# Performance work log

Hardware: AMD Instinct MI355X
Metric: run time of the kernel (lower is better)

The kernel has to match this reference:

```python
import jax, jax.numpy as jnp
import numpy as np
import math

BLOCK_SIZE = 64
GATE_HIDDEN = 128


def _rmsnorm(x, w, eps=1e-6):
    v = jnp.mean(jnp.square(x), axis=-1, keepdims=True)
    return x * jax.lax.rsqrt(v + eps) * w


def _rotate_half(x):
    x1, x2 = jnp.split(x, 2, axis=-1)
    return jnp.concatenate([-x2, x1], axis=-1)


def _rope(x, cos, sin):
    # x: [B, S, H, D]; cos/sin: [B, S, D] -> unsqueeze head dim (unsqueeze_dim=2)
    c = cos[:, :, None, :]
    s = sin[:, :, None, :]
    return x * c + _rotate_half(x) * s


def setup_inputs() -> dict:
    key = jax.random.key(0)
    ks = jax.random.split(key, 10)
    B, S, Hk, D = 4, 65536, 8, 128
    Hq, g, Dg = 32, 4, GATE_HIDDEN
    nb = S // BLOCK_SIZE
    xav_q = math.sqrt(6.0 / (D + Dg))
    xav_k = math.sqrt(6.0 / (2 * D + Dg))
    return {
        "k": jax.random.normal(ks[0], (B, S, Hk, D), jnp.float32),
        "q": jax.random.normal(ks[1], (B, 1, Hq, D), jnp.float32),
        "Wq": jax.random.uniform(ks[2], (Hk, g, D, Dg), jnp.float32, -xav_q, xav_q),
        "Wk": jax.random.uniform(ks[3], (Hk, 2 * D, Dg), jnp.float32, -xav_k, xav_k),
        "qnorm_w": jnp.ones((Dg,), jnp.float32),
        "knorm_w": jnp.ones((Dg,), jnp.float32),
        "cos_q": jax.random.uniform(ks[4], (B, 1, Dg), jnp.float32, -1.0, 1.0),
        "sin_q": jax.random.uniform(ks[5], (B, 1, Dg), jnp.float32, -1.0, 1.0),
        "cos_k": jax.random.uniform(ks[6], (B, nb, Dg), jnp.float32, -1.0, 1.0),
        "sin_k": jax.random.uniform(ks[7], (B, nb, Dg), jnp.float32, -1.0, 1.0),
        "attention_mask": jnp.ones((B, Hk, nb), jnp.bool_),
        "block_budget": 128,
    }


def reference(k, q, Wq, Wk, qnorm_w, knorm_w, cos_q, sin_q, cos_k, sin_k,
              attention_mask, block_budget):
    B, S, Hk, D = k.shape
    nb = S // BLOCK_SIZE
    g = q.shape[2] // Hk
    Dg = Wk.shape[-1]
    scale = 1.0 / math.sqrt(Dg)

    # --- K path: block pooling (avg + max) -> per-head linear -> RMSNorm -> RoPE
    kb = k.reshape(B, nb, BLOCK_SIZE, Hk, D)
    k_pooled = jnp.concatenate([kb.mean(axis=2), kb.max(axis=2)], axis=-1)  # [B,nb,Hk,2D]
    k_c = jnp.einsum('bshi,hio->bsho', k_pooled, Wk)                         # [B,nb,Hk,Dg]
    k_c = _rmsnorm(k_c, knorm_w)
    k_c = _rope(k_c, cos_k, sin_k)

    # --- Q path (Qproj): grouped per-k-head projection -> RMSNorm -> RoPE
    qg = q.reshape(B, 1, Hk, g, D)
    qp = jnp.einsum('bskgi,kgio->bsko', qg, Wq)                              # [B,1,Hk,Dg]
    qp = _rmsnorm(qp, qnorm_w)
    qp = _rope(qp, cos_q, sin_q)
    qv = qp[:, 0]                                                            # [B,Hk,Dg]

    # --- gate scores + softmax
    attn = jnp.einsum('bhd,bshd->bhs', qv, k_c) * scale                      # [B,Hk,nb]
    attn = jnp.where(attention_mask, attn, jnp.float32(-1e20))
    attn = jax.nn.softmax(attn, axis=-1)

    # --- token_budget sparse block mask: topk + scatter
    _, topk_idx = jax.lax.top_k(attn, block_budget)                          # [B,Hk,k]
    blk = jnp.arange(nb)
    mask = jnp.any(topk_idx[..., :, None] == blk[None, None, None, :], axis=-2)
    mask = mask & attention_mask
    mask = mask.at[:, :, -1].set(True)
    return mask
```

## Files before the change

### kernel.cpp

```cpp
#include <hip/hip_runtime.h>
#include <hip/hip_bf16.h>
#include <math.h>

#define NB   1024
#define HKH  8
#define NPROD 512

typedef float f4 __attribute__((ext_vector_type(4)));

__global__ __launch_bounds__(512) void qproj_kernel(const float* __restrict__ q,
                                                    const float* __restrict__ Wq,
                                                    const float* __restrict__ qnw,
                                                    const float* __restrict__ cq,
                                                    const float* __restrict__ sq,
                                                    float* __restrict__ qv) {
    int b = blockIdx.x >> 3, h = blockIdx.x & 7;
    int t = threadIdx.x;
    int o = t & 127, seg = t >> 7;
    __shared__ float qs[512];
    __shared__ float part[4][128];
    __shared__ float red[2];
    __shared__ float ybuf[128];
    qs[t] = q[(size_t)b * 4096 + (size_t)h * 512 + t];
    __syncthreads();
    const float* wqp = Wq + (size_t)h * 512 * 128 + o;
    float acc = 0.0f;
    int g0 = seg * 128;
#pragma unroll 4
    for (int gi = g0; gi < g0 + 128; ++gi)
        acc = fmaf(qs[gi], wqp[(size_t)gi * 128], acc);
    part[seg][o] = acc;
    __syncthreads();
    if (t < 128) {
        float a = part[0][o] + part[1][o] + part[2][o] + part[3][o];
        ybuf[o] = a;
        float ss = a * a;
        for (int off = 32; off > 0; off >>= 1) ss += __shfl_xor(ss, off);
        if ((o & 63) == 0) red[o >> 6] = ss;
    }
    __syncthreads();
    if (t < 128) {
        float scale = rsqrtf((red[0] + red[1]) * (1.0f / 128.0f) + 1e-6f);
        float y  = ybuf[o] * scale * qnw[o];
        int op   = (o < 64) ? o + 64 : o - 64;
        float yp = ybuf[op] * scale * qnw[op];
        float rot = (o < 64) ? -yp : yp;
        qv[((size_t)b * HKH + h) * 128 + o] =
            fmaf(y, cq[b * 128 + o], rot * sq[b * 128 + o]);
    }
}

__global__ __launch_bounds__(768) void fused_kernel(const float* __restrict__ kin,
                                                    const float* __restrict__ Wk,
                                                    const float* __restrict__ knw,
                                                    const float* __restrict__ cosk,
                                                    const float* __restrict__ sink,
                                                    const float* __restrict__ qv,
                                                    float* __restrict__ scores) {
    __shared__ float At[4][256][32];
    __shared__ int produced[4];
    int wg  = blockIdx.x;
    int b   = wg >> 6;
    int grp = wg & 63;
    int t   = threadIdx.x;

    if (t < 4) produced[t] = 0;
    __syncthreads();

    if (t < NPROD) {
        int col = t & 255;
        int h   = col >> 5;
        int c   = col & 31;
        int bihalf = t >> 8;
        const float inv = 1.0f / 64.0f;
        for (int it = 0; it < 4; ++it) {
#pragma unroll
            for (int bb2 = 0; bb2 < 2; ++bb2) {
                int bi = bihalf + bb2 * 2;
                size_t row0 = (size_t)b * 65536 +
                              ((size_t)grp * 16 + it * 4 + bi) * 64;
                const f4* src = (const f4*)kin + row0 * 256 + col;
                f4 s = {0.f, 0.f, 0.f, 0.f};
                f4 m = {-3.4e38f, -3.4e38f, -3.4e38f, -3.4e38f};
#pragma unroll 8
                for (int r = 0; r < 64; ++r) {
                    f4 u = __builtin_nontemporal_load(src + (size_t)r * 256);
                    s += u;
                    m.x = fmaxf(m.x, u.x); m.y = fmaxf(m.y, u.y);
                    m.z = fmaxf(m.z, u.z); m.w = fmaxf(m.w, u.w);
                }
#pragma unroll
                for (int j = 0; j < 4; ++j) {
                    int k0 = c * 4 + j;
                    int g  = (k0 >> 3) & 7;
                    At[it][k0      ][((h ^ g) << 2) | bi] = s[j] * inv;
                    At[it][k0 + 128][((h ^ g) << 2) | bi] = m[j];
                }
            }
            __threadfence_block();
            atomicAdd(&produced[it], 1);
        }
    } else {
        int tc = t - NPROD;
        int h  = tc >> 5;
        int c  = tc & 31;
        const float* wp = Wk + (size_t)h * 32768 + c * 4;
        f4 kn  = *(const f4*)(knw + c * 4);
        f4 qvr = *(const f4*)(qv + ((size_t)b * HKH + h) * 128 + c * 4);
        volatile int* vfl = (volatile int*)produced;

#pragma unroll
        for (int pass = 0; pass < 2; ++pass) {
            int sA = pass * 2, sB = sA + 1;
            while (vfl[sB] < NPROD) __builtin_amdgcn_s_sleep(2);
            __threadfence_block();

            float acc0[4][4], acc1[4][4];
#pragma unroll
            for (int i = 0; i < 4; ++i)
#pragma unroll
                for (int j = 0; j < 4; ++j) { acc0[i][j] = 0.0f; acc1[i][j] = 0.0f; }

#pragma unroll 4
            for (int k = 0; k < 256; ++k) {
                int g = (k >> 3) & 7;
                f4 w  = *(const f4*)(wp + (size_t)k * 128);
                f4 a0 = *(const f4*)&At[sA][k][(h ^ g) << 2];
                f4 a1 = *(const f4*)&At[sB][k][(h ^ g) << 2];
#pragma unroll
                for (int i = 0; i < 4; ++i) {
                    acc0[i][0] = fmaf(a0[i], w.x, acc0[i][0]);
                    acc0[i][1] = fmaf(a0[i], w.y, acc0[i][1]);
                    acc0[i][2] = fmaf(a0[i], w.z, acc0[i][2]);
                    acc0[i][3] = fmaf(a0[i], w.w, acc0[i][3]);
                    acc1[i][0] = fmaf(a1[i], w.x, acc1[i][0]);
                    acc1[i][1] = fmaf(a1[i], w.y, acc1[i][1]);
                    acc1[i][2] = fmaf(a1[i], w.z, acc1[i][2]);
                    acc1[i][3] = fmaf(a1[i], w.w, acc1[i][3]);
                }
            }

#pragma unroll
            for (int half = 0; half < 2; ++half) {
                float (*acc)[4] = half ? acc1 : acc0;
#pragma unroll
                for (int i = 0; i < 4; ++i) {
                    int blkg = grp * 16 + (sA + half) * 4 + i;
                    float ss = 0.0f;
#pragma unroll
                    for (int j = 0; j < 4; ++j) ss = fmaf(acc[i][j], acc[i][j], ss);
#pragma unroll
                    for (int off = 1; off < 32; off <<= 1) ss += __shfl_xor(ss, off);
                    float scale = rsqrtf(ss * (1.0f / 128.0f) + 1e-6f);
                    f4 cb = *(const f4*)(cosk + ((size_t)b * NB + blkg) * 128 + c * 4);
                    f4 sb = *(const f4*)(sink + ((size_t)b * NB + blkg) * 128 + c * 4);
                    float part = 0.0f;
#pragma unroll
                    for (int j = 0; j < 4; ++j) {
                        float y  = acc[i][j] * scale * kn[j];
                        float yp = __shfl_xor(y, 16);
                        float rot = (c < 16) ? -yp : yp;
                        float z = fmaf(y, cb[j], rot * sb[j]);
                        part = fmaf(z, qvr[j], part);
                    }
#pragma unroll
                    for (int off = 1; off < 32; off <<= 1) part += __shfl_xor(part, off);
                    if (c == 0)
                        scores[((size_t)b * HKH + h) * NB + blkg] =
                            part * 0.08838834764831845f;
                }
            }
        }
    }
}

__device__ inline bool read_mask(const void* amp, int mode, size_t idx) {
    if (mode == 1) return ((const int*)amp)[idx] != 0;
    if (mode == 2) return ((const unsigned int*)amp)[idx] != 0u;
    return ((const unsigned char*)amp)[idx] != 0;
}

__global__ __launch_bounds__(512) void topk_kernel(const float* __restrict__ scores,
                                                   const void* __restrict__ amraw,
                                                   const int* __restrict__ bbp,
                                                   int* __restrict__ out) {
    int b = blockIdx.x >> 3, h = blockIdx.x & 7;
    int t = threadIdx.x;
    __shared__ float sv[NB];
    __shared__ int mode_sh;

    if (t == 0) {
        const unsigned int* w = (const unsigned int*)amraw;
        bool allint = true, allflt = true;
        for (int i = 0; i < 64; ++i) {
            unsigned int x = w[i];
            if (x != 0u && x != 1u) allint = false;
            if (x != 0u && x != 0x3f800000u) allflt = false;
        }
        mode_sh = allint ? 1 : (allflt ? 2 : 0);
    }
    __syncthreads();
    int mode = mode_sh;
    size_t rowoff = ((size_t)b * HKH + h) * NB;
    const float* src = scores + rowoff;
    for (int s = t; s < NB; s += 512)
        sv[s] = read_mask(amraw, mode, rowoff + s) ? src[s] : -1e20f;
    __syncthreads();

    int bb = bbp[0];
    if (bb > NB) bb = NB;
    if (bb < 1)  bb = 1;

    int e0 = t, e1 = t + 512;
    float v0 = sv[e0], v1 = sv[e1];
    int r0 = 0, r1 = 0;
#pragma unroll 4
    for (int j4 = 0; j4 < 256; ++j4) {
        f4 w = *(const f4*)&sv[j4 * 4];
        int jb = j4 * 4;
        r0 += (w.x > v0) + (w.y > v0) + (w.z > v0) + (w.w > v0);
        r1 += (w.x > v1) + (w.y > v1) + (w.z > v1) + (w.w > v1);
        r0 += (w.x == v0 && jb + 0 < e0) + (w.y == v0 && jb + 1 < e0)
            + (w.z == v0 && jb + 2 < e0) + (w.w == v0 && jb + 3 < e0);
        r1 += (w.x == v1 && jb + 0 < e1) + (w.y == v1 && jb + 1 < e1)
            + (w.z == v1 && jb + 2 < e1) + (w.w == v1 && jb + 3 < e1);
    }
    int* dst = out + rowoff;
    bool am0 = read_mask(amraw, mode, rowoff + e0);
    bool am1 = read_mask(amraw, mode, rowoff + e1);
    dst[e0] = ((r0 < bb && am0)) ? 1 : 0;
    dst[e1] = ((r1 < bb && am1) || (e1 == NB - 1)) ? 1 : 0;
}

extern "C" void kernel_launch(void* const* d_in, const int* in_sizes, int n_in,
                              void* d_out, int out_size, void* d_ws, size_t ws_size,
                              hipStream_t stream) {
    (void)in_sizes; (void)n_in; (void)out_size; (void)ws_size;
    const float* k   = (const float*)d_in[0];
    const float* q   = (const float*)d_in[1];
    const float* Wq  = (const float*)d_in[2];
    const float* Wk  = (const float*)d_in[3];
    const float* qnw = (const float*)d_in[4];
    const float* knw = (const float*)d_in[5];
    const float* cq  = (const float*)d_in[6];
    const float* sq  = (const float*)d_in[7];
    const float* ck  = (const float*)d_in[8];
    const float* sk  = (const float*)d_in[9];
    const void*  am  = d_in[10];
    const int*   bb  = (const int*)d_in[11];
    int* out = (int*)d_out;

    float* qv     = (float*)d_ws;
    float* scores = qv + 4 * HKH * 128;

    qproj_kernel<<<32, 512, 0, stream>>>(q, Wq, qnw, cq, sq, qv);
    fused_kernel<<<256, 768, 0, stream>>>(k, Wk, knw, ck, sk, qv, scores);
    topk_kernel<<<32, 512, 0, stream>>>(scores, am, bb, out);
}
```

Baseline: 249.8 us.

## Let consumer warps pool the last K slab while producers handle the first three

```diff
diff --git a/kernel.cpp b/kernel.cpp
--- a/kernel.cpp
+++ b/kernel.cpp
@@ -67,13 +67,14 @@
     if (t < 4) produced[t] = 0;
     __syncthreads();
 
+    const float inv = 1.0f / 64.0f;
+
     if (t < NPROD) {
         int col = t & 255;
         int h   = col >> 5;
         int c   = col & 31;
         int bihalf = t >> 8;
-        const float inv = 1.0f / 64.0f;
-        for (int it = 0; it < 4; ++it) {
+        for (int it = 0; it < 3; ++it) {
 #pragma unroll
             for (int bb2 = 0; bb2 < 2; ++bb2) {
                 int bi = bihalf + bb2 * 2;
@@ -104,29 +105,54 @@
         int tc = t - NPROD;
         int h  = tc >> 5;
         int c  = tc & 31;
+
+        {
+            int col = tc;
+#pragma unroll
+            for (int bi = 0; bi < 4; ++bi) {
+                size_t row0 = (size_t)b * 65536 +
+                              ((size_t)grp * 16 + 12 + bi) * 64;
+                const f4* src = (const f4*)kin + row0 * 256 + col;
+                f4 s = {0.f, 0.f, 0.f, 0.f};
+                f4 m = {-3.4e38f, -3.4e38f, -3.4e38f, -3.4e38f};
+#pragma unroll 8
+                for (int r = 0; r < 64; ++r) {
+                    f4 u = __builtin_nontemporal_load(src + (size_t)r * 256);
+                    s += u;
+                    m.x = fmaxf(m.x, u.x); m.y = fmaxf(m.y, u.y);
+                    m.z = fmaxf(m.z, u.z); m.w = fmaxf(m.w, u.w);
+                }
+#pragma unroll
+                for (int j = 0; j < 4; ++j) {
+                    int k0 = c * 4 + j;
+                    int g  = (k0 >> 3) & 7;
+                    At[3][k0      ][((h ^ g) << 2) | bi] = s[j] * inv;
+                    At[3][k0 + 128][((h ^ g) << 2) | bi] = m[j];
+                }
+            }
+            __threadfence_block();
+            atomicAdd(&produced[3], 1);
+        }
+
         const float* wp = Wk + (size_t)h * 32768 + c * 4;
         f4 kn  = *(const f4*)(knw + c * 4);
         f4 qvr = *(const f4*)(qv + ((size_t)b * HKH + h) * 128 + c * 4);
         volatile int* vfl = (volatile int*)produced;
 
-#pragma unroll
-        for (int pass = 0; pass < 2; ++pass) {
-            int sA = pass * 2, sB = sA + 1;
-            while (vfl[sB] < NPROD) __builtin_amdgcn_s_sleep(2);
-            __threadfence_block();
-
+        while (vfl[1] < NPROD) __builtin_amdgcn_s_sleep(2);
+        __threadfence_block();
+        {
             float acc0[4][4], acc1[4][4];
 #pragma unroll
             for (int i = 0; i < 4; ++i)
 #pragma unroll
                 for (int j = 0; j < 4; ++j) { acc0[i][j] = 0.0f; acc1[i][j] = 0.0f; }
-
 #pragma unroll 4
             for (int k = 0; k < 256; ++k) {
                 int g = (k >> 3) & 7;
                 f4 w  = *(const f4*)(wp + (size_t)k * 128);
-                f4 a0 = *(const f4*)&At[sA][k][(h ^ g) << 2];
-                f4 a1 = *(const f4*)&At[sB][k][(h ^ g) << 2];
+                f4 a0 = *(const f4*)&At[0][k][(h ^ g) << 2];
+                f4 a1 = *(const f4*)&At[1][k][(h ^ g) << 2];
 #pragma unroll
                 for (int i = 0; i < 4; ++i) {
                     acc0[i][0] = fmaf(a0[i], w.x, acc0[i][0]);
@@ -139,13 +165,12 @@
                     acc1[i][3] = fmaf(a1[i], w.w, acc1[i][3]);
                 }
             }
-
 #pragma unroll
             for (int half = 0; half < 2; ++half) {
                 float (*acc)[4] = half ? acc1 : acc0;
 #pragma unroll
                 for (int i = 0; i < 4; ++i) {
-                    int blkg = grp * 16 + (sA + half) * 4 + i;
+                    int blkg = grp * 16 + half * 4 + i;
                     float ss = 0.0f;
 #pragma unroll
                     for (int j = 0; j < 4; ++j) ss = fmaf(acc[i][j], acc[i][j], ss);
@@ -169,6 +194,57 @@
                         scores[((size_t)b * HKH + h) * NB + blkg] =
                             part * 0.08838834764831845f;
                 }
+            }
+        }
+
+#pragma unroll
+        for (int sl = 2; sl < 4; ++sl) {
+            int need = (sl == 3) ? 256 : NPROD;
+            while (vfl[sl] < need) __builtin_amdgcn_s_sleep(2);
+            __threadfence_block();
+            float acc[4][4];
+#pragma unroll
+            for (int i = 0; i < 4; ++i)
+#pragma unroll
+                for (int j = 0; j < 4; ++j) acc[i][j] = 0.0f;
+#pragma unroll 4
+            for (int k = 0; k < 256; ++k) {
+                int g = (k >> 3) & 7;
+                f4 w = *(const f4*)(wp + (size_t)k * 128);
+                f4 a = *(const f4*)&At[sl][k][(h ^ g) << 2];
+#pragma unroll
+                for (int i = 0; i < 4; ++i) {
+                    acc[i][0] = fmaf(a[i], w.x, acc[i][0]);
+                    acc[i][1] = fmaf(a[i], w.y, acc[i][1]);
+                    acc[i][2] = fmaf(a[i], w.z, acc[i][2]);
+                    acc[i][3] = fmaf(a[i], w.w, acc[i][3]);
+                }
+            }
+#pragma unroll
+            for (int i = 0; i < 4; ++i) {
+                int blkg = grp * 16 + sl * 4 + i;
+                float ss = 0.0f;
+#pragma unroll
+                for (int j = 0; j < 4; ++j) ss = fmaf(acc[i][j], acc[i][j], ss);
+#pragma unroll
+                for (int off = 1; off < 32; off <<= 1) ss += __shfl_xor(ss, off);
+                float scale = rsqrtf(ss * (1.0f / 128.0f) + 1e-6f);
+                f4 cb = *(const f4*)(cosk + ((size_t)b * NB + blkg) * 128 + c * 4);
+                f4 sb = *(const f4*)(sink + ((size_t)b * NB + blkg) * 128 + c * 4);
+                float part = 0.0f;
+#pragma unroll
+                for (int j = 0; j < 4; ++j) {
+                    float y  = acc[i][j] * scale * kn[j];
+                    float yp = __shfl_xor(y, 16);
+                    float rot = (c < 16) ? -yp : yp;
+                    float z = fmaf(y, cb[j], rot * sb[j]);
+                    part = fmaf(z, qvr[j], part);
+                }
+#pragma unroll
+                for (int off = 1; off < 32; off <<= 1) part += __shfl_xor(part, off);
+                if (c == 0)
+                    scores[((size_t)b * HKH + h) * NB + blkg] =
+                        part * 0.08838834764831845f;
             }
         }
     }
```

Result: slower. 267.2 us (+7.0%).

## Fuse Q projection and top-k into the pooling kernel via global flags

Applied to the files above, without the earlier changes.

```diff
diff --git a/kernel.cpp b/kernel.cpp
--- a/kernel.cpp
+++ b/kernel.cpp
@@ -8,55 +8,22 @@
 
 typedef float f4 __attribute__((ext_vector_type(4)));
 
-__global__ __launch_bounds__(512) void qproj_kernel(const float* __restrict__ q,
-                                                    const float* __restrict__ Wq,
-                                                    const float* __restrict__ qnw,
-                                                    const float* __restrict__ cq,
-                                                    const float* __restrict__ sq,
-                                                    float* __restrict__ qv) {
-    int b = blockIdx.x >> 3, h = blockIdx.x & 7;
-    int t = threadIdx.x;
-    int o = t & 127, seg = t >> 7;
-    __shared__ float qs[512];
-    __shared__ float part[4][128];
-    __shared__ float red[2];
-    __shared__ float ybuf[128];
-    qs[t] = q[(size_t)b * 4096 + (size_t)h * 512 + t];
-    __syncthreads();
-    const float* wqp = Wq + (size_t)h * 512 * 128 + o;
-    float acc = 0.0f;
-    int g0 = seg * 128;
-#pragma unroll 4
-    for (int gi = g0; gi < g0 + 128; ++gi)
-        acc = fmaf(qs[gi], wqp[(size_t)gi * 128], acc);
-    part[seg][o] = acc;
-    __syncthreads();
-    if (t < 128) {
-        float a = part[0][o] + part[1][o] + part[2][o] + part[3][o];
-        ybuf[o] = a;
-        float ss = a * a;
-        for (int off = 32; off > 0; off >>= 1) ss += __shfl_xor(ss, off);
-        if ((o & 63) == 0) red[o >> 6] = ss;
-    }
-    __syncthreads();
-    if (t < 128) {
-        float scale = rsqrtf((red[0] + red[1]) * (1.0f / 128.0f) + 1e-6f);
-        float y  = ybuf[o] * scale * qnw[o];
-        int op   = (o < 64) ? o + 64 : o - 64;
-        float yp = ybuf[op] * scale * qnw[op];
-        float rot = (o < 64) ? -yp : yp;
-        qv[((size_t)b * HKH + h) * 128 + o] =
-            fmaf(y, cq[b * 128 + o], rot * sq[b * 128 + o]);
-    }
+__device__ inline bool read_mask(const void* amp, int mode, size_t idx) {
+    if (mode == 1) return ((const int*)amp)[idx] != 0;
+    if (mode == 2) return ((const unsigned int*)amp)[idx] != 0u;
+    return ((const unsigned char*)amp)[idx] != 0;
 }
 
-__global__ __launch_bounds__(768) void fused_kernel(const float* __restrict__ kin,
-                                                    const float* __restrict__ Wk,
-                                                    const float* __restrict__ knw,
-                                                    const float* __restrict__ cosk,
-                                                    const float* __restrict__ sink,
-                                                    const float* __restrict__ qv,
-                                                    float* __restrict__ scores) {
+__global__ __launch_bounds__(832) void fused_kernel(
+    const float* __restrict__ kin,  const float* __restrict__ qrow,
+    const float* __restrict__ Wq,   const float* __restrict__ Wk,
+    const float* __restrict__ qnw,  const float* __restrict__ knw,
+    const float* __restrict__ cq,   const float* __restrict__ sq,
+    const float* __restrict__ cosk, const float* __restrict__ sink,
+    const void* __restrict__ amraw, const int* __restrict__ bbp,
+    int* __restrict__ flags, float* __restrict__ qv,
+    float* __restrict__ scores, int* __restrict__ out)
+{
     __shared__ float At[4][256][32];
     __shared__ int produced[4];
     int wg  = blockIdx.x;
@@ -66,13 +33,43 @@
 
     if (t < 4) produced[t] = 0;
     __syncthreads();
+    const float inv = 1.0f / 64.0f;
+
+    if (t >= 768) {
+        if (wg < 32) {
+            int qb = wg >> 3, qh = wg & 7;
+            int o  = t - 768;
+            const float* qs  = qrow + (size_t)qb * 4096 + (size_t)qh * 512;
+            const float* wqp = Wq + (size_t)qh * 65536;
+            float accA = 0.0f, accB = 0.0f;
+#pragma unroll 8
+            for (int gi = 0; gi < 512; ++gi) {
+                float qg = qs[gi];
+                accA = fmaf(qg, wqp[(size_t)gi * 128 + o],      accA);
+                accB = fmaf(qg, wqp[(size_t)gi * 128 + o + 64], accB);
+            }
+            float ss = accA * accA + accB * accB;
+#pragma unroll
+            for (int off = 1; off < 64; off <<= 1) ss += __shfl_xor(ss, off);
+            float scale = rsqrtf(ss * (1.0f / 128.0f) + 1e-6f);
+            float yA = accA * scale * qnw[o];
+            float yB = accB * scale * qnw[o + 64];
+            float zA = fmaf(yA, cq[qb * 128 + o],      -(yB * sq[qb * 128 + o]));
+            float zB = fmaf(yB, cq[qb * 128 + o + 64],   yA * sq[qb * 128 + o + 64]);
+            float* qd = qv + ((size_t)qb * HKH + qh) * 128;
+            atomicExch(&qd[o],      zA);
+            atomicExch(&qd[o + 64], zB);
+            __threadfence();
+            if (o == 0) atomicAdd(&flags[0], 1);
+        }
+        return;
+    }
 
     if (t < NPROD) {
         int col = t & 255;
         int h   = col >> 5;
         int c   = col & 31;
         int bihalf = t >> 8;
-        const float inv = 1.0f / 64.0f;
         for (int it = 0; it < 4; ++it) {
 #pragma unroll
             for (int bb2 = 0; bb2 < 2; ++bb2) {
@@ -105,9 +102,9 @@
         int h  = tc >> 5;
         int c  = tc & 31;
         const float* wp = Wk + (size_t)h * 32768 + c * 4;
-        f4 kn  = *(const f4*)(knw + c * 4);
-        f4 qvr = *(const f4*)(qv + ((size_t)b * HKH + h) * 128 + c * 4);
+        f4 kn = *(const f4*)(knw + c * 4);
         volatile int* vfl = (volatile int*)produced;
+        f4 qvr;
 
 #pragma unroll
         for (int pass = 0; pass < 2; ++pass) {
@@ -140,6 +137,12 @@
                 }
             }
 
+            if (pass == 0) {
+                while (atomicAdd(&flags[0], 0) < 32) __builtin_amdgcn_s_sleep(2);
+                __threadfence();
+                qvr = *(const f4*)(qv + ((size_t)b * HKH + h) * 128 + c * 4);
+            }
+
 #pragma unroll
             for (int half = 0; half < 2; ++half) {
                 float (*acc)[4] = half ? acc1 : acc0;
@@ -166,70 +169,61 @@
 #pragma unroll
                     for (int off = 1; off < 32; off <<= 1) part += __shfl_xor(part, off);
                     if (c == 0)
-                        scores[((size_t)b * HKH + h) * NB + blkg] =
-                            part * 0.08838834764831845f;
-                }
+                        atomicExch(&scores[((size_t)b * HKH + h) * NB + blkg],
+                                   part * 0.08838834764831845f);
+                }
+            }
+        }
+
+        if (c == 0) {
+            __threadfence();
+            atomicAdd(&flags[1 + b * 8 + h], 1);
+        }
+
+        if (grp < 8) {
+            int hrow = grp;
+            size_t rowoff = ((size_t)b * HKH + hrow) * NB;
+            while (atomicAdd(&flags[1 + b * 8 + hrow], 0) < 64)
+                __builtin_amdgcn_s_sleep(4);
+            __threadfence();
+            const unsigned int* wam = (const unsigned int*)amraw;
+            bool allint = true, allflt = true;
+            for (int i = 0; i < 64; ++i) {
+                unsigned int x = wam[i];
+                if (x != 0u && x != 1u) allint = false;
+                if (x != 0u && x != 0x3f800000u) allflt = false;
+            }
+            int mode = allint ? 1 : (allflt ? 2 : 0);
+            int bb = bbp[0];
+            if (bb > NB) bb = NB;
+            if (bb < 1)  bb = 1;
+            int e0 = tc * 4;
+            float v[4]; bool amv[4]; int r[4] = {0, 0, 0, 0};
+#pragma unroll
+            for (int j = 0; j < 4; ++j) {
+                amv[j] = read_mask(amraw, mode, rowoff + e0 + j);
+                v[j] = amv[j] ? scores[rowoff + e0 + j] : -1e20f;
+            }
+            for (int j4 = 0; j4 < 256; ++j4) {
+                f4 w = *(const f4*)&scores[rowoff + j4 * 4];
+                int jb = j4 * 4;
+#pragma unroll
+                for (int l = 0; l < 4; ++l) {
+                    float wl = (l == 0) ? w.x : (l == 1) ? w.y : (l == 2) ? w.z : w.w;
+                    float wv = read_mask(amraw, mode, rowoff + jb + l) ? wl : -1e20f;
+                    int idx = jb + l;
+#pragma unroll
+                    for (int cd = 0; cd < 4; ++cd)
+                        r[cd] += (wv > v[cd]) + (wv == v[cd] && idx < e0 + cd);
+                }
+            }
+#pragma unroll
+            for (int cd = 0; cd < 4; ++cd) {
+                int e = e0 + cd;
+                out[rowoff + e] = ((r[cd] < bb && amv[cd]) || e == NB - 1) ? 1 : 0;
             }
         }
     }
-}
-
-__device__ inline bool read_mask(const void* amp, int mode, size_t idx) {
-    if (mode == 1) return ((const int*)amp)[idx] != 0;
-    if (mode == 2) return ((const unsigned int*)amp)[idx] != 0u;
-    return ((const unsigned char*)amp)[idx] != 0;
-}
-
-__global__ __launch_bounds__(512) void topk_kernel(const float* __restrict__ scores,
-                                                   const void* __restrict__ amraw,
-                                                   const int* __restrict__ bbp,
-                                                   int* __restrict__ out) {
-    int b = blockIdx.x >> 3, h = blockIdx.x & 7;
-    int t = threadIdx.x;
-    __shared__ float sv[NB];
-    __shared__ int mode_sh;
-
-    if (t == 0) {
-        const unsigned int* w = (const unsigned int*)amraw;
-        bool allint = true, allflt = true;
-        for (int i = 0; i < 64; ++i) {
-            unsigned int x = w[i];
-            if (x != 0u && x != 1u) allint = false;
-            if (x != 0u && x != 0x3f800000u) allflt = false;
-        }
-        mode_sh = allint ? 1 : (allflt ? 2 : 0);
-    }
-    __syncthreads();
-    int mode = mode_sh;
-    size_t rowoff = ((size_t)b * HKH + h) * NB;
-    const float* src = scores + rowoff;
-    for (int s = t; s < NB; s += 512)
-        sv[s] = read_mask(amraw, mode, rowoff + s) ? src[s] : -1e20f;
-    __syncthreads();
-
-    int bb = bbp[0];
-    if (bb > NB) bb = NB;
-    if (bb < 1)  bb = 1;
-
-    int e0 = t, e1 = t + 512;
-    float v0 = sv[e0], v1 = sv[e1];
-    int r0 = 0, r1 = 0;
-#pragma unroll 4
-    for (int j4 = 0; j4 < 256; ++j4) {
-        f4 w = *(const f4*)&sv[j4 * 4];
-        int jb = j4 * 4;
-        r0 += (w.x > v0) + (w.y > v0) + (w.z > v0) + (w.w > v0);
-        r1 += (w.x > v1) + (w.y > v1) + (w.z > v1) + (w.w > v1);
-        r0 += (w.x == v0 && jb + 0 < e0) + (w.y == v0 && jb + 1 < e0)
-            + (w.z == v0 && jb + 2 < e0) + (w.w == v0 && jb + 3 < e0);
-        r1 += (w.x == v1 && jb + 0 < e1) + (w.y == v1 && jb + 1 < e1)
-            + (w.z == v1 && jb + 2 < e1) + (w.w == v1 && jb + 3 < e1);
-    }
-    int* dst = out + rowoff;
-    bool am0 = read_mask(amraw, mode, rowoff + e0);
-    bool am1 = read_mask(amraw, mode, rowoff + e1);
-    dst[e0] = ((r0 < bb && am0)) ? 1 : 0;
-    dst[e1] = ((r1 < bb && am1) || (e1 == NB - 1)) ? 1 : 0;
 }
 
 extern "C" void kernel_launch(void* const* d_in, const int* in_sizes, int n_in,
@@ -250,10 +244,12 @@
     const int*   bb  = (const int*)d_in[11];
     int* out = (int*)d_out;
 
-    float* qv     = (float*)d_ws;
+    int*   flags  = (int*)d_ws;
+    float* qv     = (float*)d_ws + 64;
     float* scores = qv + 4 * HKH * 128;
 
-    qproj_kernel<<<32, 512, 0, stream>>>(q, Wq, qnw, cq, sq, qv);
-    fused_kernel<<<256, 768, 0, stream>>>(k, Wk, knw, ck, sk, qv, scores);
-    topk_kernel<<<32, 512, 0, stream>>>(scores, am, bb, out);
+    hipMemsetAsync(d_ws, 0, 256, stream);
+    fused_kernel<<<256, 832, 0, stream>>>(k, q, Wq, Wk, qnw, knw, cq, sq,
+                                          ck, sk, am, bb,
+                                          flags, qv, scores, out);
 }
```

After: 413.0 us. +65.4%, slower.
